# Kernel optimization log

Measured on AMD Instinct MI355X. Metric: run time of the kernel, lower is better.

The kernel has to match this reference:

```python
import jax, jax.numpy as jnp
import numpy as np

ALPHA = 8.3  # depth similarity sharpness, F_D = exp(-alpha*|D(p0)-D(pn)|) (depth-aware CNN)
PAD, STRIDE, DIL, KH, KW = 1, 1, 1, 3, 3


def setup_inputs() -> dict:
    key = jax.random.key(0)
    k1, k2, k3, k4 = jax.random.split(key, 4)
    B, C_in, C_out, H, W = 2, 32, 32, 512, 512
    x = jax.random.normal(k1, (B, C_in, H, W), dtype=jnp.float32)
    depth = jax.random.uniform(k2, (B, 1, H, W), dtype=jnp.float32)
    weight = jax.random.normal(k3, (C_out, C_in, KH, KW), dtype=jnp.float32) * 0.05
    bias = jax.random.normal(k4, (C_out,), dtype=jnp.float32) * 0.05
    return {"x": x, "depth": depth, "weight": weight, "bias": bias}


def _depthconv(x, depth, weight, bias):
    B, C, H, W = x.shape
    C_out = weight.shape[0]
    H_out = (H + 2 * PAD - DIL * (KH - 1) - 1) // STRIDE + 1
    W_out = (W + 2 * PAD - DIL * (KW - 1) - 1) // STRIDE + 1
    x_p = jnp.pad(x, ((0, 0), (0, 0), (PAD, PAD), (PAD, PAD)))
    d_p = jnp.pad(depth, ((0, 0), (0, 0), (PAD, PAD), (PAD, PAD)))
    # depth at the receptive-field center of each output pixel, [B,1,H_out,W_out]
    ci, cj = (KH // 2) * DIL, (KW // 2) * DIL
    d_c = d_p[:, :, ci:ci + H_out * STRIDE:STRIDE, cj:cj + W_out * STRIDE:STRIDE]
    out = jnp.broadcast_to(bias[None, :, None, None], (B, C_out, H_out, W_out)).astype(x.dtype)
    for ki in range(KH):
        for kj in range(KW):
            hs, ws = ki * DIL, kj * DIL
            xs = x_p[:, :, hs:hs + H_out * STRIDE:STRIDE, ws:ws + W_out * STRIDE:STRIDE]
            ds = d_p[:, :, hs:hs + H_out * STRIDE:STRIDE, ws:ws + W_out * STRIDE:STRIDE]
            sim = jnp.exp(-ALPHA * jnp.abs(d_c - ds))  # [B,1,H_out,W_out]
            out = out + jnp.einsum('oc,bchw->bohw', weight[:, :, ki, kj], xs * sim)
    return out


def reference(x, depth, weight, bias):
    return _depthconv(x, depth, weight, bias)
```

## Files before the change

kernel.cpp:

```cpp
#include <hip/hip_runtime.h>
#include <hip/hip_bf16.h>

typedef short short8 __attribute__((ext_vector_type(8)));
typedef float floatx4 __attribute__((ext_vector_type(4)));

constexpr int C  = 32, H = 512, W = 512, HW = H * W;
constexpr int Hp = 514, Wp = 514;
constexpr int NPX = 2 * Hp * Wp;

constexpr size_t XOFF = 0;
constexpr size_t XSZ  = (size_t)NPX * 64;
constexpr size_t DOFF = XOFF + XSZ;
constexpr size_t DSZ  = (size_t)NPX * 8;
constexpr size_t WOFF = DOFF + DSZ;

__device__ __forceinline__ unsigned short bf16u(float f) {
    return __builtin_bit_cast(unsigned short, __float2bfloat16(f));
}
__device__ __forceinline__ unsigned pack2(float lo, float hi) {
    return (unsigned)bf16u(lo) | ((unsigned)bf16u(hi) << 16);
}

__global__ __launch_bounds__(256) void pack_x(const float* __restrict__ x,
                                              unsigned* __restrict__ xp) {
    __shared__ float t[C][65];
    const int bid = blockIdx.x;
    const int wseg = bid & 7, h = (bid >> 3) & 511, b = bid >> 12;
    const int w0 = wseg * 64;
    const int tid = threadIdx.x;

    const float* xb = x + (size_t)b * C * HW + h * W + w0;
    #pragma unroll
    for (int p = 0; p < 2; ++p) {
        int c = p * 16 + (tid >> 4), f4 = tid & 15;
        float4 v = *(const float4*)(xb + (size_t)c * HW + f4 * 4);
        t[c][f4 * 4 + 0] = v.x; t[c][f4 * 4 + 1] = v.y;
        t[c][f4 * 4 + 2] = v.z; t[c][f4 * 4 + 3] = v.w;
    }
    __syncthreads();

    const int px = tid >> 2, q = tid & 3;
    uint4 o;
    o.x = pack2(t[q * 8 + 0][px], t[q * 8 + 1][px]);
    o.y = pack2(t[q * 8 + 2][px], t[q * 8 + 3][px]);
    o.z = pack2(t[q * 8 + 4][px], t[q * 8 + 5][px]);
    o.w = pack2(t[q * 8 + 6][px], t[q * 8 + 7][px]);
    size_t ppx = ((size_t)(b * Hp + h + 1)) * Wp + (w0 + 1 + px);
    *(uint4*)(xp + ppx * 16 + q * 4) = o;
}

__global__ __launch_bounds__(256) void pack_d(const float* __restrict__ depth,
                                              float2* __restrict__ dpk) {
    int gid = blockIdx.x * 256 + threadIdx.x;
    int b = gid >> 18, hw = gid & (HW - 1), h = hw >> 9, w = hw & 511;
    float d = depth[gid];
    size_t ppx = ((size_t)(b * Hp + h + 1)) * Wp + (w + 1);
    dpk[ppx] = make_float2(__expf(-8.3f * d), __expf(8.3f * d));
}

__global__ __launch_bounds__(256) void pack_border(unsigned* __restrict__ xp,
                                                   float2* __restrict__ dpk) {
    int i = blockIdx.x * 256 + threadIdx.x;
    if (i >= 4104) return;
    int b = i / 2052, r = i % 2052;
    int hh, ww;
    if (r < 514)       { hh = 0;   ww = r; }
    else if (r < 1028) { hh = 513; ww = r - 514; }
    else { int j = r - 1028; hh = 1 + (j >> 1); ww = (j & 1) ? 513 : 0; }
    size_t ppx = ((size_t)(b * Hp + hh)) * Wp + ww;
    uint4 z = {0u, 0u, 0u, 0u};
    uint4* p = (uint4*)(xp + ppx * 16);
    p[0] = z; p[1] = z; p[2] = z; p[3] = z;
    dpk[ppx] = make_float2(0.f, 0.f);
}

__global__ __launch_bounds__(256) void pack_w(const float* __restrict__ weight,
                                              uint4* __restrict__ wp) {
    int i = blockIdx.x * 256 + threadIdx.x;
    if (i >= 1152) return;
    int lane = i & 63, half = (i >> 6) & 1, tap = i >> 7;
    int o = half * 16 + (lane & 15), q = lane >> 4;
    uint4 v;
    unsigned pk[4];
    #pragma unroll
    for (int p = 0; p < 4; ++p) {
        float lo = weight[(o * 32 + q * 8 + 2 * p) * 9 + tap];
        float hi = weight[(o * 32 + q * 8 + 2 * p + 1) * 9 + tap];
        pk[p] = pack2(lo, hi);
    }
    v.x = pk[0]; v.y = pk[1]; v.z = pk[2]; v.w = pk[3];
    wp[i] = v;
}

__global__ __launch_bounds__(256) void depthconv_main(
    const unsigned* __restrict__ xp,
    const float2*   __restrict__ dpk,
    const uint4*    __restrict__ wp,
    const float*    __restrict__ bias,
    float*          __restrict__ out)
{
    const int bid  = blockIdx.x;
    const int wseg = bid & 7, h = (bid >> 3) & 511, b = bid >> 12;
    const int lane = threadIdx.x & 63, wid = threadIdx.x >> 6;
    const int nn   = lane & 15, q = lane >> 4;
    const int pw   = wseg * 64 + wid * 16 + nn;

    short8 af[2][9];
    #pragma unroll
    for (int tap = 0; tap < 9; ++tap) {
        af[0][tap] = __builtin_bit_cast(short8, wp[(tap * 2 + 0) * 64 + lane]);
        af[1][tap] = __builtin_bit_cast(short8, wp[(tap * 2 + 1) * 64 + lane]);
    }

    floatx4 acc0, acc1;
    #pragma unroll
    for (int r = 0; r < 4; ++r) {
        acc0[r] = bias[q * 4 + r];
        acc1[r] = bias[16 + q * 4 + r];
    }

    const size_t rowbase = ((size_t)(b * Hp + h)) * Wp + pw;
    const float2 dc = dpk[rowbase + Wp + 1];

    #pragma unroll
    for (int ki = 0; ki < 3; ++ki) {
        #pragma unroll
        for (int kj = 0; kj < 3; ++kj) {
            const int tap = ki * 3 + kj;
            const size_t np = rowbase + (size_t)ki * Wp + kj;
            float2 dn = dpk[np];
            float s = fminf(dn.y * dc.x, dn.x * dc.y);

            const uint4 xv = *(const uint4*)(xp + np * 16 + q * 4);
            const unsigned uu[4] = { xv.x, xv.y, xv.z, xv.w };
            unsigned pk[4];
            #pragma unroll
            for (int p = 0; p < 4; ++p) {
                unsigned u = uu[p];
                float lo = __builtin_bit_cast(float, u << 16) * s;
                float hi = __builtin_bit_cast(float, u & 0xffff0000u) * s;
                pk[p] = pack2(lo, hi);
            }
            short8 bfrag = __builtin_bit_cast(short8, *(const uint4*)pk);

            acc0 = __builtin_amdgcn_mfma_f32_16x16x32_bf16(af[0][tap], bfrag, acc0, 0, 0, 0);
            acc1 = __builtin_amdgcn_mfma_f32_16x16x32_bf16(af[1][tap], bfrag, acc1, 0, 0, 0);
        }
    }

    float* op = out + (size_t)b * C * HW + h * W + pw;
    #pragma unroll
    for (int r = 0; r < 4; ++r) {
        op[(size_t)(q * 4 + r) * HW]        = acc0[r];
        op[(size_t)(16 + q * 4 + r) * HW]   = acc1[r];
    }
}

extern "C" void kernel_launch(void* const* d_in, const int* in_sizes, int n_in,
                              void* d_out, int out_size, void* d_ws, size_t ws_size,
                              hipStream_t stream) {
    const float* x      = (const float*)d_in[0];
    const float* depth  = (const float*)d_in[1];
    const float* weight = (const float*)d_in[2];
    const float* bias   = (const float*)d_in[3];
    float* out          = (float*)d_out;

    unsigned* xp  = (unsigned*)((char*)d_ws + XOFF);
    float2*   dpk = (float2*)  ((char*)d_ws + DOFF);
    uint4*    wpk = (uint4*)   ((char*)d_ws + WOFF);

    hipLaunchKernelGGL(pack_x,      dim3(2 * 512 * 8), dim3(256), 0, stream, x, xp);
    hipLaunchKernelGGL(pack_d,      dim3(2 * HW / 256), dim3(256), 0, stream, depth, dpk);
    hipLaunchKernelGGL(pack_border, dim3(17),           dim3(256), 0, stream, xp, dpk);
    hipLaunchKernelGGL(pack_w,      dim3(5),            dim3(256), 0, stream, weight, wpk);
    hipLaunchKernelGGL(depthconv_main, dim3(2 * 512 * 8), dim3(256), 0, stream,
                       xp, dpk, wpk, bias, out);
}
```

Baseline: 166.7 us.

## Switch to fp16 MFMA with packed-half scaling and fuse pack kernels

Replaces bf16 storage and MFMA with fp16. The per-tap depth-similarity scaling becomes a packed half multiply instead of unpacking to float, multiplying and repacking. The four pre-pack kernels (x, depth, border, weights) are merged into one launch, and each x-packing block now handles four rows. This cuts the per-tap VALU work in the main kernel and removes three launches, but fp16 has less range than bf16, and the larger shared tile in the pack kernel may lower occupancy.

```diff
diff --git a/kernel.cpp b/kernel.cpp
--- a/kernel.cpp
+++ b/kernel.cpp
@@ -1,7 +1,6 @@
 #include <hip/hip_runtime.h>
-#include <hip/hip_bf16.h>
 
-typedef short short8 __attribute__((ext_vector_type(8)));
+typedef _Float16 half8 __attribute__((ext_vector_type(8)));
 typedef float floatx4 __attribute__((ext_vector_type(4)));
 
 constexpr int C  = 32, H = 512, W = 512, HW = H * W;
@@ -14,82 +13,82 @@
 constexpr size_t DSZ  = (size_t)NPX * 8;
 constexpr size_t WOFF = DOFF + DSZ;
 
-__device__ __forceinline__ unsigned short bf16u(float f) {
-    return __builtin_bit_cast(unsigned short, __float2bfloat16(f));
-}
-__device__ __forceinline__ unsigned pack2(float lo, float hi) {
-    return (unsigned)bf16u(lo) | ((unsigned)bf16u(hi) << 16);
+__device__ __forceinline__ unsigned pack2h(float lo, float hi) {
+    unsigned a = (unsigned)__builtin_bit_cast(unsigned short, (_Float16)lo);
+    unsigned b = (unsigned)__builtin_bit_cast(unsigned short, (_Float16)hi);
+    return a | (b << 16);
 }
 
-__global__ __launch_bounds__(256) void pack_x(const float* __restrict__ x,
-                                              unsigned* __restrict__ xp) {
-    __shared__ float t[C][65];
+__global__ __launch_bounds__(256) void pack_all(
+    const float* __restrict__ x, const float* __restrict__ depth,
+    const float* __restrict__ weight,
+    unsigned* __restrict__ xp, float2* __restrict__ dpk, uint4* __restrict__ wp)
+{
     const int bid = blockIdx.x;
-    const int wseg = bid & 7, h = (bid >> 3) & 511, b = bid >> 12;
-    const int w0 = wseg * 64;
     const int tid = threadIdx.x;
 
-    const float* xb = x + (size_t)b * C * HW + h * W + w0;
+    if (bid >= 2048) {
+        if (bid < 2065) {
+            int i = (bid - 2048) * 256 + tid;
+            if (i >= 4104) return;
+            int b = i / 2052, r = i % 2052;
+            int hh, ww;
+            if (r < 514)       { hh = 0;   ww = r; }
+            else if (r < 1028) { hh = 513; ww = r - 514; }
+            else { int j = r - 1028; hh = 1 + (j >> 1); ww = (j & 1) ? 513 : 0; }
+            size_t ppx = ((size_t)(b * Hp + hh)) * Wp + ww;
+            uint4 z = {0u, 0u, 0u, 0u};
+            uint4* p = (uint4*)(xp + ppx * 16);
+            p[0] = z; p[1] = z; p[2] = z; p[3] = z;
+            dpk[ppx] = make_float2(0.f, 0.f);
+        } else {
+            int j = (bid - 2065) * 256 + tid;
+            if (j >= 1152) return;
+            int lane = j & 63, half = (j >> 6) & 1, tap = j >> 7;
+            int o = half * 16 + (lane & 15), q = lane >> 4;
+            uint4 v;
+            v.x = pack2h(weight[(o * 32 + q * 8 + 0) * 9 + tap], weight[(o * 32 + q * 8 + 1) * 9 + tap]);
+            v.y = pack2h(weight[(o * 32 + q * 8 + 2) * 9 + tap], weight[(o * 32 + q * 8 + 3) * 9 + tap]);
+            v.z = pack2h(weight[(o * 32 + q * 8 + 4) * 9 + tap], weight[(o * 32 + q * 8 + 5) * 9 + tap]);
+            v.w = pack2h(weight[(o * 32 + q * 8 + 6) * 9 + tap], weight[(o * 32 + q * 8 + 7) * 9 + tap]);
+            wp[j] = v;
+        }
+        return;
+    }
+
+    __shared__ float t[4][32][65];
+    const int wseg = bid & 7, hseg = (bid >> 3) & 127, b = bid >> 10;
+    const int h0 = hseg * 4, w0 = wseg * 64;
+
+    const float* xb = x + (size_t)b * C * HW + h0 * W + w0;
     #pragma unroll
-    for (int p = 0; p < 2; ++p) {
-        int c = p * 16 + (tid >> 4), f4 = tid & 15;
-        float4 v = *(const float4*)(xb + (size_t)c * HW + f4 * 4);
-        t[c][f4 * 4 + 0] = v.x; t[c][f4 * 4 + 1] = v.y;
-        t[c][f4 * 4 + 2] = v.z; t[c][f4 * 4 + 3] = v.w;
+    for (int p = 0; p < 8; ++p) {
+        int slot = p * 256 + tid;
+        int r = slot >> 9, c = (slot >> 4) & 31, f4 = slot & 15;
+        float4 v = *(const float4*)(xb + (size_t)c * HW + r * W + f4 * 4);
+        t[r][c][f4 * 4 + 0] = v.x; t[r][c][f4 * 4 + 1] = v.y;
+        t[r][c][f4 * 4 + 2] = v.z; t[r][c][f4 * 4 + 3] = v.w;
+    }
+
+    {
+        int rr = tid >> 6, ww = tid & 63;
+        float d = depth[(size_t)b * HW + (h0 + rr) * W + w0 + ww];
+        size_t ppx = ((size_t)(b * Hp + h0 + rr + 1)) * Wp + (w0 + 1 + ww);
+        dpk[ppx] = make_float2(__expf(-8.3f * d), __expf(8.3f * d));
     }
     __syncthreads();
 
     const int px = tid >> 2, q = tid & 3;
-    uint4 o;
-    o.x = pack2(t[q * 8 + 0][px], t[q * 8 + 1][px]);
-    o.y = pack2(t[q * 8 + 2][px], t[q * 8 + 3][px]);
-    o.z = pack2(t[q * 8 + 4][px], t[q * 8 + 5][px]);
-    o.w = pack2(t[q * 8 + 6][px], t[q * 8 + 7][px]);
-    size_t ppx = ((size_t)(b * Hp + h + 1)) * Wp + (w0 + 1 + px);
-    *(uint4*)(xp + ppx * 16 + q * 4) = o;
-}
-
-__global__ __launch_bounds__(256) void pack_d(const float* __restrict__ depth,
-                                              float2* __restrict__ dpk) {
-    int gid = blockIdx.x * 256 + threadIdx.x;
-    int b = gid >> 18, hw = gid & (HW - 1), h = hw >> 9, w = hw & 511;
-    float d = depth[gid];
-    size_t ppx = ((size_t)(b * Hp + h + 1)) * Wp + (w + 1);
-    dpk[ppx] = make_float2(__expf(-8.3f * d), __expf(8.3f * d));
-}
-
-__global__ __launch_bounds__(256) void pack_border(unsigned* __restrict__ xp,
-                                                   float2* __restrict__ dpk) {
-    int i = blockIdx.x * 256 + threadIdx.x;
-    if (i >= 4104) return;
-    int b = i / 2052, r = i % 2052;
-    int hh, ww;
-    if (r < 514)       { hh = 0;   ww = r; }
-    else if (r < 1028) { hh = 513; ww = r - 514; }
-    else { int j = r - 1028; hh = 1 + (j >> 1); ww = (j & 1) ? 513 : 0; }
-    size_t ppx = ((size_t)(b * Hp + hh)) * Wp + ww;
-    uint4 z = {0u, 0u, 0u, 0u};
-    uint4* p = (uint4*)(xp + ppx * 16);
-    p[0] = z; p[1] = z; p[2] = z; p[3] = z;
-    dpk[ppx] = make_float2(0.f, 0.f);
-}
-
-__global__ __launch_bounds__(256) void pack_w(const float* __restrict__ weight,
-                                              uint4* __restrict__ wp) {
-    int i = blockIdx.x * 256 + threadIdx.x;
-    if (i >= 1152) return;
-    int lane = i & 63, half = (i >> 6) & 1, tap = i >> 7;
-    int o = half * 16 + (lane & 15), q = lane >> 4;
-    uint4 v;
-    unsigned pk[4];
     #pragma unroll
-    for (int p = 0; p < 4; ++p) {
-        float lo = weight[(o * 32 + q * 8 + 2 * p) * 9 + tap];
-        float hi = weight[(o * 32 + q * 8 + 2 * p + 1) * 9 + tap];
-        pk[p] = pack2(lo, hi);
+    for (int r = 0; r < 4; ++r) {
+        uint4 o;
+        o.x = pack2h(t[r][q * 8 + 0][px], t[r][q * 8 + 1][px]);
+        o.y = pack2h(t[r][q * 8 + 2][px], t[r][q * 8 + 3][px]);
+        o.z = pack2h(t[r][q * 8 + 4][px], t[r][q * 8 + 5][px]);
+        o.w = pack2h(t[r][q * 8 + 6][px], t[r][q * 8 + 7][px]);
+        size_t ppx = ((size_t)(b * Hp + h0 + r + 1)) * Wp + (w0 + 1 + px);
+        *(uint4*)(xp + ppx * 16 + q * 4) = o;
     }
-    v.x = pk[0]; v.y = pk[1]; v.z = pk[2]; v.w = pk[3];
-    wp[i] = v;
 }
 
 __global__ __launch_bounds__(256) void depthconv_main(
@@ -105,11 +104,11 @@
     const int nn   = lane & 15, q = lane >> 4;
     const int pw   = wseg * 64 + wid * 16 + nn;
 
-    short8 af[2][9];
+    half8 af[2][9];
     #pragma unroll
     for (int tap = 0; tap < 9; ++tap) {
-        af[0][tap] = __builtin_bit_cast(short8, wp[(tap * 2 + 0) * 64 + lane]);
-        af[1][tap] = __builtin_bit_cast(short8, wp[(tap * 2 + 1) * 64 + lane]);
+        af[0][tap] = __builtin_bit_cast(half8, wp[(tap * 2 + 0) * 64 + lane]);
+        af[1][tap] = __builtin_bit_cast(half8, wp[(tap * 2 + 1) * 64 + lane]);
     }
 
     floatx4 acc0, acc1;
@@ -130,21 +129,14 @@
             const size_t np = rowbase + (size_t)ki * Wp + kj;
             float2 dn = dpk[np];
             float s = fminf(dn.y * dc.x, dn.x * dc.y);
+            _Float16 hs = (_Float16)s;
+            half8 sv = { hs, hs, hs, hs, hs, hs, hs, hs };
 
-            const uint4 xv = *(const uint4*)(xp + np * 16 + q * 4);
-            const unsigned uu[4] = { xv.x, xv.y, xv.z, xv.w };
-            unsigned pk[4];
-            #pragma unroll
-            for (int p = 0; p < 4; ++p) {
-                unsigned u = uu[p];
-                float lo = __builtin_bit_cast(float, u << 16) * s;
-                float hi = __builtin_bit_cast(float, u & 0xffff0000u) * s;
-                pk[p] = pack2(lo, hi);
-            }
-            short8 bfrag = __builtin_bit_cast(short8, *(const uint4*)pk);
+            half8 xv = __builtin_bit_cast(half8, *(const uint4*)(xp + np * 16 + q * 4));
+            half8 bfrag = xv * sv;
 
-            acc0 = __builtin_amdgcn_mfma_f32_16x16x32_bf16(af[0][tap], bfrag, acc0, 0, 0, 0);
-            acc1 = __builtin_amdgcn_mfma_f32_16x16x32_bf16(af[1][tap], bfrag, acc1, 0, 0, 0);
+            acc0 = __builtin_amdgcn_mfma_f32_16x16x32_f16(af[0][tap], bfrag, acc0, 0, 0, 0);
+            acc1 = __builtin_amdgcn_mfma_f32_16x16x32_f16(af[1][tap], bfrag, acc1, 0, 0, 0);
         }
     }
 
@@ -169,10 +161,8 @@
     float2*   dpk = (float2*)  ((char*)d_ws + DOFF);
     uint4*    wpk = (uint4*)   ((char*)d_ws + WOFF);
 
-    hipLaunchKernelGGL(pack_x,      dim3(2 * 512 * 8), dim3(256), 0, stream, x, xp);
-    hipLaunchKernelGGL(pack_d,      dim3(2 * HW / 256), dim3(256), 0, stream, depth, dpk);
-    hipLaunchKernelGGL(pack_border, dim3(17),           dim3(256), 0, stream, xp, dpk);
-    hipLaunchKernelGGL(pack_w,      dim3(5),            dim3(256), 0, stream, weight, wpk);
+    hipLaunchKernelGGL(pack_all, dim3(2070), dim3(256), 0, stream,
+                       x, depth, weight, xp, dpk, wpk);
     hipLaunchKernelGGL(depthconv_main, dim3(2 * 512 * 8), dim3(256), 0, stream,
                        xp, dpk, wpk, bias, out);
 }
```

After: 160.1 us. 1.04x faster.
